# Kernel optimization log

Hardware: AMD Instinct MI355X
Metric: run time of the kernel (lower is better)

## Reference

```python
import jax, jax.numpy as jnp
import numpy as np

IN_DIM = 768
OUT_DIM = 4096
N_SK_ITER = 3
TARGET_TEMP = 0.06
PRED_TEMP = 0.12
PREFACTOR = 1.0
EXP_MAX = 50.0  # exp_max_values[float32]
SK_EPS = 1e-8
NORM_EPS = 1e-7


def setup_inputs() -> dict:
    key = jax.random.key(0)
    kx, kw = jax.random.split(key)
    x = jax.random.normal(kx, (16, 1024, IN_DIM), dtype=jnp.float32)
    # nn.Linear weight init: normal(std=1); bias zeros
    weight = jax.random.normal(kw, (OUT_DIM, IN_DIM), dtype=jnp.float32)
    bias = jnp.zeros((OUT_DIM,), dtype=jnp.float32)
    return {"x": x, "weight": weight, "bias": bias}


def sinkhorn_knopp(M, n_iterations, eps=SK_EPS):
    # stable_exp: shift by max over dim=-2 (token axis), add EXP_MAX
    shift = jnp.max(M, axis=-2, keepdims=True)
    M = jnp.exp(M + EXP_MAX - shift)
    for _ in range(n_iterations):  # small fixed count
        M = M / (jnp.sum(M, axis=-2, keepdims=True) + eps)  # column normalize
        M = M / (jnp.sum(M, axis=-1, keepdims=True) + eps)  # row normalize
    return M


def reference(x, weight, bias):
    # L2 normalize features (eps matches torch F.normalize with p=2)
    norm = jnp.maximum(jnp.linalg.norm(x, axis=-1, keepdims=True), NORM_EPS)
    x_n = x / norm
    logits = jnp.einsum("bnd,kd->bnk", x_n, weight) + bias  # [B, N, K]
    # positionwise_sk=True: no flatten before sinkhorn; detach -> stop_gradient
    assignments = sinkhorn_knopp(jax.lax.stop_gradient(logits) / TARGET_TEMP, N_SK_ITER)
    tgt = assignments.reshape(-1, OUT_DIM).astype(jnp.float32)
    pred = logits.reshape(-1, OUT_DIM).astype(jnp.float32)
    loss = -jnp.mean(jnp.sum(tgt * jax.nn.log_softmax(pred / PRED_TEMP, axis=-1), axis=-1))
    return assignments, PREFACTOR * loss
```

## Files before the change

kernel.cpp:

```cpp
#include <hip/hip_runtime.h>
#include <math.h>

#define BATCH 16
#define NTOK  1024
#define NCLU  4096
#define DIM   768
#define MROWS (BATCH * NTOK)

constexpr float TT_INV    = 16.666666666666668f;
constexpr float PT_INV    = 8.333333333333334f;
constexpr float SK_EPS_   = 1e-8f;
constexpr float NORM_EPS_ = 1e-7f;
constexpr float COL_SHIFT = 60.0f;
constexpr float P_SHIFT   = 40.0f;

typedef _Float16 f16x8 __attribute__((ext_vector_type(8)));
typedef _Float16 f16x4 __attribute__((ext_vector_type(4)));
typedef float    f32x4 __attribute__((ext_vector_type(4)));

struct F8 { float v[8]; };

__device__ __forceinline__ F8 load8(const float* p) {
    const float4 a = *(const float4*)p;
    const float4 b = *(const float4*)(p + 4);
    return F8{{a.x, a.y, a.z, a.w, b.x, b.y, b.z, b.w}};
}
__device__ __forceinline__ F8 load8(const _Float16* p) {
    f16x8 h = *(const f16x8*)p;
    F8 r;
#pragma unroll
    for (int i = 0; i < 8; ++i) r.v[i] = (float)h[i];
    return r;
}

__device__ __forceinline__ float wave_sum(float s) {
#pragma unroll
    for (int off = 32; off; off >>= 1) s += __shfl_xor(s, off);
    return s;
}

__device__ __forceinline__ void gl_lds16(const void* g, void* l) {
    __builtin_amdgcn_global_load_lds(
        (const __attribute__((address_space(1))) unsigned int*)g,
        (__attribute__((address_space(3))) unsigned int*)l,
        16, 0, 0);
}

__global__ __launch_bounds__(256) void castx_kernel(
    const float* __restrict__ x, _Float16* __restrict__ x16)
{
    int row  = (blockIdx.x * 256 + threadIdx.x) >> 6;
    int lane = threadIdx.x & 63;
    const float4* rp = (const float4*)(x + (size_t)row * DIM);
    float4 v[3];
    float ss = 0.f;
#pragma unroll
    for (int i = 0; i < 3; ++i) {
        v[i] = rp[lane + i * 64];
        ss += v[i].x * v[i].x + v[i].y * v[i].y + v[i].z * v[i].z + v[i].w * v[i].w;
    }
    ss = wave_sum(ss);
    float sc = 1.0f / fmaxf(sqrtf(ss), NORM_EPS_);
    _Float16* op = x16 + (size_t)row * DIM;
#pragma unroll
    for (int i = 0; i < 3; ++i) {
        f16x4 h;
        h[0] = (_Float16)(v[i].x * sc); h[1] = (_Float16)(v[i].y * sc);
        h[2] = (_Float16)(v[i].z * sc); h[3] = (_Float16)(v[i].w * sc);
        *(f16x4*)(op + 4 * (lane + i * 64)) = h;
    }
}

__global__ __launch_bounds__(256) void castw_kernel(
    const float* __restrict__ w, _Float16* __restrict__ w16)
{
    int i = blockIdx.x * 256 + threadIdx.x;
    const float4 a = *(const float4*)(w + (size_t)i * 8);
    const float4 b = *(const float4*)(w + (size_t)i * 8 + 4);
    f16x8 h;
    h[0] = (_Float16)a.x; h[1] = (_Float16)a.y; h[2] = (_Float16)a.z; h[3] = (_Float16)a.w;
    h[4] = (_Float16)b.x; h[5] = (_Float16)b.y; h[6] = (_Float16)b.z; h[7] = (_Float16)b.w;
    *(f16x8*)(w16 + (size_t)i * 8) = h;
}

__global__ __launch_bounds__(256) void rownorm_kernel(
    const float* __restrict__ x, float* __restrict__ invn)
{
    int wave = (blockIdx.x * 256 + threadIdx.x) >> 6;
    int lane = threadIdx.x & 63;
    const float4* row = (const float4*)(x + (size_t)wave * DIM);
    float s = 0.f;
#pragma unroll
    for (int i = 0; i < 3; ++i) {
        float4 v = row[lane + i * 64];
        s += v.x * v.x + v.y * v.y + v.z * v.z + v.w * v.w;
    }
    s = wave_sum(s);
    if (lane == 0) invn[wave] = 1.0f / fmaxf(sqrtf(s), NORM_EPS_);
}

#define GKH   32
#define NKH   (DIM / GKH)

__global__ void __launch_bounds__(512, 1) gemm16(
    const _Float16* __restrict__ A,
    const _Float16* __restrict__ B,
    const float* __restrict__ bias,
    _Float16* __restrict__ out,
    float* __restrict__ colpart)
{
    __shared__ __align__(16) _Float16 AS[4][8192];
    __shared__ __align__(16) _Float16 BS[4][8192];

    const int tid  = threadIdx.x;
    const int lane = tid & 63;
    const int wid  = tid >> 6;
    const int wm   = wid >> 2;
    const int wn   = wid & 3;

    const int nwg = gridDim.x;
    const int cpx = nwg >> 3;
    const int swz = (blockIdx.x & 7) * cpx + (blockIdx.x >> 3);
    const int brow = (swz >> 4) * 256;
    const int bcol = (swz & 15) * 256;

    const int G0 = tid, G1 = tid + 512;
    const int pr0 = G0 >> 3, s0 = G0 & 7;
    const int rr0 = pr0 * 2 + (s0 >> 2), qq0 = (s0 & 3) ^ (pr0 & 3);
    const int pr1 = G1 >> 3, s1 = G1 & 7;
    const int rr1 = pr1 * 2 + (s1 >> 2), qq1 = (s1 & 3) ^ (pr1 & 3);

    const _Float16* sA0 = A + (size_t)(brow + rr0) * DIM + qq0 * 8;
    const _Float16* sA1 = A + (size_t)(brow + rr1) * DIM + qq1 * 8;
    const _Float16* sB0 = B + (size_t)(bcol + rr0) * DIM + qq0 * 8;
    const _Float16* sB1 = B + (size_t)(bcol + rr1) * DIM + qq1 * 8;
    const int ldsOff0 = wid * 512;
    const int ldsOff1 = wid * 512 + 4096;

    const int q  = lane >> 4;
    const int fr = lane & 15;
    const int qp = q ^ ((fr >> 1) & 3);
    const int fbase = ((fr & 1) * 4 + qp) * 8;
    const int abase = (wm * 64 + (fr >> 1)) * 64 + fbase;
    const int bbase = (wn * 32 + (fr >> 1)) * 64 + fbase;

    f32x4 acc[8][4] = {};

#define STAGE4(slot, kh) {                                  \
    const int ko_ = (kh) * GKH;                             \
    gl_lds16(sA0 + ko_, &AS[slot][ldsOff0]);                \
    gl_lds16(sA1 + ko_, &AS[slot][ldsOff1]);                \
    gl_lds16(sB0 + ko_, &BS[slot][ldsOff0]);                \
    gl_lds16(sB1 + ko_, &BS[slot][ldsOff1]); }

#define PHASE(slotC, slotS, khS) {                                         \
    STAGE4(slotS, khS);                                                    \
    asm volatile("s_waitcnt vmcnt(8)" ::: "memory");                       \
    __builtin_amdgcn_s_barrier();                                          \
    asm volatile("" ::: "memory");                                         \
    f16x8 af[8], bf[4];                                                    \
    _Pragma("unroll")                                                      \
    for (int m = 0; m < 8; ++m)                                            \
        af[m] = *(const f16x8*)&AS[slotC][abase + m * 512];                \
    _Pragma("unroll")                                                      \
    for (int n = 0; n < 4; ++n)                                            \
        bf[n] = *(const f16x8*)&BS[slotC][bbase + n * 512];                \
    __builtin_amdgcn_s_setprio(1);                                         \
    _Pragma("unroll")                                                      \
    for (int m = 0; m < 8; ++m)                                            \
        _Pragma("unroll")                                                  \
        for (int n = 0; n < 4; ++n)                                        \
            acc[m][n] = __builtin_amdgcn_mfma_f32_16x16x32_f16(            \
                af[m], bf[n], acc[m][n], 0, 0, 0);                         \
    __builtin_amdgcn_s_setprio(0); }

    STAGE4(0, 0);
    STAGE4(1, 1);

    for (int i6 = 0; i6 < 6; ++i6) {
        const int i = i6 * 4;
        const int kh2 = i + 2;
        const int kh3 = i + 3;
        const int kh4 = (i + 4 < NKH) ? i + 4 : i + 4 - NKH;
        const int kh5 = (i + 5 < NKH) ? i + 5 : i + 5 - NKH;
        PHASE(0, 2, kh2);
        PHASE(1, 3, kh3);
        PHASE(2, 0, kh4);
        PHASE(3, 1, kh5);
    }
#undef PHASE
#undef STAGE4

    __syncthreads();

    float cs[4] = {0.f, 0.f, 0.f, 0.f};
    float bv[4];
#pragma unroll
    for (int n = 0; n < 4; ++n) bv[n] = bias[bcol + wn * 64 + n * 16 + fr];
#pragma unroll
    for (int m = 0; m < 8; ++m) {
        int row0 = brow + wm * 128 + m * 16 + (q << 2);
#pragma unroll
        for (int j = 0; j < 4; ++j) {
            size_t ro = (size_t)(row0 + j) * NCLU + bcol + wn * 64 + fr;
#pragma unroll
            for (int n = 0; n < 4; ++n) {
                float v = acc[m][n][j] + bv[n];
                out[ro + n * 16] = (_Float16)v;
                cs[n] += __expf(v * TT_INV - COL_SHIFT);
            }
        }
    }
    float cred_local[4];
#pragma unroll
    for (int n = 0; n < 4; ++n) {
        float c2 = cs[n];
        c2 += __shfl_xor(c2, 16);
        c2 += __shfl_xor(c2, 32);
        cred_local[n] = c2;
    }
    float* cred = (float*)&AS[0][0];
#pragma unroll
    for (int n = 0; n < 4; ++n)
        if (q == 0) cred[((wm * 4 + wn) * 4 + n) * 16 + fr] = cred_local[n];
    __syncthreads();
    if (tid < 256) {
        int wn2 = tid >> 6, n2 = (tid >> 4) & 3, fr2 = tid & 15;
        float S = cred[((0 * 4 + wn2) * 4 + n2) * 16 + fr2]
                + cred[((1 * 4 + wn2) * 4 + n2) * 16 + fr2];
        colpart[(size_t)(swz >> 4) * NCLU + bcol + wn2 * 64 + n2 * 16 + fr2] = S;
    }
}

__global__ __launch_bounds__(256) void colfin_kernel(
    const float* __restrict__ part, float* __restrict__ a1)
{
    int i = blockIdx.x * 256 + threadIdx.x;
    int b = i >> 12, k = i & (NCLU - 1);
    const float* p = part + (size_t)(b * 4) * NCLU + k;
    float s = 0.f;
#pragma unroll
    for (int rb = 0; rb < 4; ++rb) { s += *p; p += NCLU; }
    a1[i] = -COL_SHIFT - __logf(s);
}

template <bool FIRST>
__global__ __launch_bounds__(256) void rcpass_kernel(
    const _Float16* __restrict__ L, const float* __restrict__ a_in,
    const float* __restrict__ b_in, float* __restrict__ b_out,
    float* __restrict__ part)
{
    __shared__ float wgt_sh[16];
    const int tid  = threadIdx.x;
    const int lane = tid & 63;
    const int wv   = tid >> 6;
    const int chunk = blockIdx.x;
    const int b     = chunk >> 6;
    const int row0  = chunk * 16;
    const float* av = a_in + (size_t)b * NCLU;

    float ar[8][8];
#pragma unroll
    for (int i = 0; i < 8; ++i) {
        int c = i * 64 + lane;
        *(float4*)&ar[i][0] = *(const float4*)&av[c * 8];
        *(float4*)&ar[i][4] = *(const float4*)&av[c * 8 + 4];
    }

#pragma unroll
    for (int rr = 0; rr < 4; ++rr) {
        int row = row0 + wv * 4 + rr;
        const _Float16* Lr = L + (size_t)row * NCLU;
        float bp = FIRST ? 0.f : b_in[row];
        float s = 0.f;
#pragma unroll
        for (int i = 0; i < 8; ++i) {
            int c = i * 64 + lane;
            f16x8 h = *(const f16x8*)&Lr[c * 8];
#pragma unroll
            for (int j = 0; j < 8; ++j)
                s += __expf((float)h[j] * TT_INV + ar[i][j] + bp);
        }
        s = wave_sum(s);
        if (lane == 0) {
            float bn = bp - __logf(s + SK_EPS_);
            b_out[row] = bn;
            wgt_sh[wv * 4 + rr] = __expf(bn);
        }
    }
    __syncthreads();

    float aown[2][8];
#pragma unroll
    for (int sl = 0; sl < 2; ++sl) {
        *(float4*)&aown[sl][0] = *(const float4*)&av[sl * 2048 + tid * 8];
        *(float4*)&aown[sl][4] = *(const float4*)&av[sl * 2048 + tid * 8 + 4];
    }
    float acc[2][8] = {};
    for (int rr = 0; rr < 16; ++rr) {
        const _Float16* Lr = L + (size_t)(row0 + rr) * NCLU;
        float wg = wgt_sh[rr];
#pragma unroll
        for (int sl = 0; sl < 2; ++sl) {
            f16x8 h = *(const f16x8*)&Lr[sl * 2048 + tid * 8];
#pragma unroll
            for (int j = 0; j < 8; ++j)
                acc[sl][j] += __expf((float)h[j] * TT_INV + aown[sl][j]) * wg;
        }
    }
    float* P = part + (size_t)chunk * NCLU;
#pragma unroll
    for (int sl = 0; sl < 2; ++sl) {
        f32x4 w0, w1;
        w0[0] = acc[sl][0]; w0[1] = acc[sl][1]; w0[2] = acc[sl][2]; w0[3] = acc[sl][3];
        w1[0] = acc[sl][4]; w1[1] = acc[sl][5]; w1[2] = acc[sl][6]; w1[3] = acc[sl][7];
        *(f32x4*)&P[sl * 2048 + tid * 8]     = w0;
        *(f32x4*)&P[sl * 2048 + tid * 8 + 4] = w1;
    }
}

__global__ __launch_bounds__(256) void colfinN_kernel(
    const float* __restrict__ part, const float* __restrict__ a_in,
    float* __restrict__ a_out)
{
    int i = blockIdx.x * 256 + threadIdx.x;
    int b = i >> 12, k = i & (NCLU - 1);
    const float* p = part + (size_t)(b * 64) * NCLU + k;
    float s = 0.f;
#pragma unroll 8
    for (int c = 0; c < 64; ++c) { s += *p; p += NCLU; }
    a_out[i] = a_in[i] - __logf(s + SK_EPS_);
}

#define BM 128
#define BN 128
#define BKF 32
#define LDK 40

__device__ __forceinline__ f16x8 pack8(float4 lo, float4 hi, float sc) {
    f16x8 h;
    h[0] = (_Float16)(lo.x * sc); h[1] = (_Float16)(lo.y * sc);
    h[2] = (_Float16)(lo.z * sc); h[3] = (_Float16)(lo.w * sc);
    h[4] = (_Float16)(hi.x * sc); h[5] = (_Float16)(hi.y * sc);
    h[6] = (_Float16)(hi.z * sc); h[7] = (_Float16)(hi.w * sc);
    return h;
}

template <typename OT>
__global__ __launch_bounds__(256) void gemm_f16(
    const float* __restrict__ x, const float* __restrict__ w,
    const float* __restrict__ bias, const float* __restrict__ invn,
    OT* __restrict__ out)
{
    __shared__ __align__(16) _Float16 As[BM * LDK];
    __shared__ __align__(16) _Float16 Bs[BN * LDK];

    const int tid  = threadIdx.x;
    const int lane = tid & 63;
    const int wid  = tid >> 6;
    const int wr = wid >> 1, wc = wid & 1;
    const int brow = blockIdx.y * BM;
    const int bcol = blockIdx.x * BN;

    const int r0 = tid >> 2;
    const int r1 = r0 + 64;
    const int kc = (tid & 3) * 8;
    const float sA0 = invn[brow + r0];
    const float sA1 = invn[brow + r1];
    const float* gA0 = x + (size_t)(brow + r0) * DIM + kc;
    const float* gA1 = x + (size_t)(brow + r1) * DIM + kc;
    const float* gB0 = w + (size_t)(bcol + r0) * DIM + kc;
    const float* gB1 = w + (size_t)(bcol + r1) * DIM + kc;

    f32x4 acc[4][4] = {};
    float4 a00, a01, a10, a11, b00, b01, b10, b11;
    a00 = *(const float4*)(gA0);     a01 = *(const float4*)(gA0 + 4);
    a10 = *(const float4*)(gA1);     a11 = *(const float4*)(gA1 + 4);
    b00 = *(const float4*)(gB0);     b01 = *(const float4*)(gB0 + 4);
    b10 = *(const float4*)(gB1);     b11 = *(const float4*)(gB1 + 4);

    const int NT = DIM / BKF;
    for (int kt = 0; kt < NT; ++kt) {
        __syncthreads();
        *(f16x8*)&As[r0 * LDK + kc] = pack8(a00, a01, sA0);
        *(f16x8*)&As[r1 * LDK + kc] = pack8(a10, a11, sA1);
        *(f16x8*)&Bs[r0 * LDK + kc] = pack8(b00, b01, 1.0f);
        *(f16x8*)&Bs[r1 * LDK + kc] = pack8(b10, b11, 1.0f);
        __syncthreads();

        if (kt + 1 < NT) {
            int k0 = (kt + 1) * BKF;
            a00 = *(const float4*)(gA0 + k0); a01 = *(const float4*)(gA0 + k0 + 4);
            a10 = *(const float4*)(gA1 + k0); a11 = *(const float4*)(gA1 + k0 + 4);
            b00 = *(const float4*)(gB0 + k0); b01 = *(const float4*)(gB0 + k0 + 4);
            b10 = *(const float4*)(gB1 + k0); b11 = *(const float4*)(gB1 + k0 + 4);
        }

        const int ko = (lane >> 4) * 8;
        f16x8 af[4], bf[4];
#pragma unroll
        for (int m = 0; m < 4; ++m)
            af[m] = *(const f16x8*)&As[(wr * 64 + m * 16 + (lane & 15)) * LDK + ko];
#pragma unroll
        for (int n = 0; n < 4; ++n)
            bf[n] = *(const f16x8*)&Bs[(wc * 64 + n * 16 + (lane & 15)) * LDK + ko];
#pragma unroll
        for (int m = 0; m < 4; ++m)
#pragma unroll
            for (int n = 0; n < 4; ++n)
                acc[m][n] = __builtin_amdgcn_mfma_f32_16x16x32_f16(
                    af[m], bf[n], acc[m][n], 0, 0, 0);
    }

#pragma unroll
    for (int n = 0; n < 4; ++n) {
        int col = bcol + wc * 64 + n * 16 + (lane & 15);
        float bv = bias[col];
#pragma unroll
        for (int m = 0; m < 4; ++m) {
            int row0 = brow + wr * 64 + m * 16 + ((lane >> 4) << 2);
#pragma unroll
            for (int j = 0; j < 4; ++j)
                out[(size_t)(row0 + j) * NCLU + col] = (OT)(acc[m][n][j] + bv);
        }
    }
}

template <typename T>
__global__ __launch_bounds__(256) void colpass_kernel(
    const T* __restrict__ L, const float* __restrict__ a_in,
    const float* __restrict__ b_in, float* __restrict__ a_out)
{
    __shared__ float bsh[NTOK];
    __shared__ float ss[4][64];
    int b = blockIdx.x >> 6;
    int k = ((blockIdx.x & 63) << 6) + (threadIdx.x & 63);
    int wv = threadIdx.x >> 6;
    int lane = threadIdx.x & 63;
    const bool first = (b_in == nullptr);
    if (first) {
        for (int i = threadIdx.x; i < NTOK; i += 256) bsh[i] = 0.f;
    } else {
        for (int i = threadIdx.x; i < NTOK; i += 256) bsh[i] = b_in[b * NTOK + i];
    }
    __syncthreads();
    float aval = first ? -COL_SHIFT : a_in[b * NCLU + k];
    const T* p = L + (size_t)b * NTOK * NCLU + (size_t)(wv * 256) * NCLU + k;
    float s = 0.f;
#pragma unroll 4
    for (int n = 0; n < 256; ++n) {
        s += __expf((float)(*p) * TT_INV + aval + bsh[wv * 256 + n]);
        p += NCLU;
    }
    ss[wv][lane] = s;
    __syncthreads();
    if (wv == 0) {
        float S = ss[0][lane] + ss[1][lane] + ss[2][lane] + ss[3][lane];
        a_out[b * NCLU + k] = aval - __logf(first ? S : S + SK_EPS_);
    }
}

template <typename T>
__global__ __launch_bounds__(256) void colpassV_kernel(
    const T* __restrict__ L, const float* __restrict__ a_in,
    const float* __restrict__ b_in, float* __restrict__ a_out)
{
    __shared__ float bsh[NTOK];
    __shared__ float red[16][16][8];
    const int b     = blockIdx.x >> 5;
    const int strip = blockIdx.x & 31;
    const int cc    = threadIdx.x & 15;
    const int rg    = threadIdx.x >> 4;
    const int col0  = strip * 128 + cc * 8;
    for (int i = threadIdx.x; i < NTOK; i += 256) bsh[i] = b_in[b * NTOK + i];
    __syncthreads();
    const float4 av0 = *(const float4*)(a_in + b * NCLU + col0);
    const float4 av1 = *(const float4*)(a_in + b * NCLU + col0 + 4);
    const float av[8] = {av0.x, av0.y, av0.z, av0.w, av1.x, av1.y, av1.z, av1.w};
    float s[8] = {};
    const T* p = L + (size_t)b * NTOK * NCLU + (size_t)rg * NCLU + col0;
    for (int it = 0; it < 64; ++it) {
        F8 Lv = load8(p);
        float bpv = bsh[it * 16 + rg];
#pragma unroll
        for (int j = 0; j < 8; ++j) s[j] += __expf(Lv.v[j] * TT_INV + av[j] + bpv);
        p += (size_t)16 * NCLU;
    }
#pragma unroll
    for (int j = 0; j < 8; ++j) red[rg][cc][j] = s[j];
    __syncthreads();
    if (threadIdx.x < 128) {
        int c2 = threadIdx.x >> 3, j2 = threadIdx.x & 7;
        float S = 0.f;
#pragma unroll
        for (int g = 0; g < 16; ++g) S += red[g][c2][j2];
        int col = strip * 128 + c2 * 8 + j2;
        a_out[b * NCLU + col] = a_in[b * NCLU + col] - __logf(S + SK_EPS_);
    }
}

template <typename T>
__global__ __launch_bounds__(256) void rowpass_kernel(
    const T* __restrict__ L, const float* __restrict__ a_in,
    const float* __restrict__ b_in, float* __restrict__ b_out)
{
    int row  = (blockIdx.x * 256 + threadIdx.x) >> 6;
    int lane = threadIdx.x & 63;
    int b = row >> 10;
    const T* Lr = L + (size_t)row * NCLU;
    const float* av = a_in + (size_t)b * NCLU;
    float bp = b_in ? b_in[row] : 0.f;
    float s = 0.f;
#pragma unroll
    for (int i = 0; i < 8; ++i) {
        int c = i * 64 + lane;
        F8 Lv = load8(Lr + c * 8);
        F8 Av = load8(av + c * 8);
#pragma unroll
        for (int j = 0; j < 8; ++j)
            s += __expf(Lv.v[j] * TT_INV + Av.v[j] + bp);
    }
    s = wave_sum(s);
    if (lane == 0) b_out[row] = bp - __logf(s + SK_EPS_);
}

template <typename T>
__global__ __launch_bounds__(256) void final_kernel(
    const T* __restrict__ L, const float* __restrict__ a3,
    const float* __restrict__ b2, float* __restrict__ out,
    float* __restrict__ rowloss)
{
    __shared__ float red[3][4];
    const int row  = blockIdx.x;
    const int tid  = threadIdx.x;
    const int lane = tid & 63;
    const int wv   = tid >> 6;
    const int b    = row >> 10;
    const T* Lr = L + (size_t)row * NCLU;
    const float* av = a3 + (size_t)b * NCLU;
    const float bp = b2[row];

    float e[2][8];
    float rs = 0.f, q = 0.f, sP = 0.f;
#pragma unroll
    for (int jj = 0; jj < 2; ++jj) {
        int c = tid + jj * 256;
        F8 Lv = load8(Lr + c * 8);
        F8 Av = load8(av + c * 8);
#pragma unroll
        for (int j = 0; j < 8; ++j) {
            float P  = Lv.v[j] * PT_INV;
            float ev = __expf(Lv.v[j] * TT_INV + Av.v[j] + bp);
            e[jj][j] = ev;
            rs += ev;
            q  += ev * P;
            sP += __expf(P - P_SHIFT);
        }
    }
    rs = wave_sum(rs); q = wave_sum(q); sP = wave_sum(sP);
    if (lane == 0) { red[0][wv] = rs; red[1][wv] = q; red[2][wv] = sP; }
    __syncthreads();
    rs = red[0][0] + red[0][1] + red[0][2] + red[0][3];
    q  = red[1][0] + red[1][1] + red[1][2] + red[1][3];
    sP = red[2][0] + red[2][1] + red[2][2] + red[2][3];

    const float inv = 1.0f / (rs + SK_EPS_);
    const float lse = P_SHIFT + __logf(sP);

    float* Or = out + (size_t)row * NCLU;
#pragma unroll
    for (int jj = 0; jj < 2; ++jj) {
        int c = tid + jj * 256;
        f32x4 w0, w1;
        w0[0] = e[jj][0] * inv; w0[1] = e[jj][1] * inv;
        w0[2] = e[jj][2] * inv; w0[3] = e[jj][3] * inv;
        w1[0] = e[jj][4] * inv; w1[1] = e[jj][5] * inv;
        w1[2] = e[jj][6] * inv; w1[3] = e[jj][7] * inv;
        __builtin_nontemporal_store(w0, (f32x4*)(Or + c * 8));
        __builtin_nontemporal_store(w1, (f32x4*)(Or + c * 8 + 4));
    }
    if (tid == 0) rowloss[row] = q * inv - lse * (rs * inv);
}

__global__ __launch_bounds__(256) void lossred_kernel(
    const float* __restrict__ rowloss, float* __restrict__ out_loss)
{
    __shared__ float red[4];
    int tid = threadIdx.x, lane = tid & 63, wv = tid >> 6;
    float s = 0.f;
    for (int i = tid; i < MROWS; i += 256) s += rowloss[i];
    s = wave_sum(s);
    if (lane == 0) red[wv] = s;
    __syncthreads();
    if (tid == 0)
        out_loss[0] = -(red[0] + red[1] + red[2] + red[3]) / (float)MROWS;
}

extern "C" void kernel_launch(void* const* d_in, const int* in_sizes, int n_in,
                              void* d_out, int out_size, void* d_ws, size_t ws_size,
                              hipStream_t stream)
{
    const float* x    = (const float*)d_in[0];
    const float* w    = (const float*)d_in[1];
    const float* bias = (const float*)d_in[2];
    float* out = (float*)d_out;
    char* base = (char*)d_ws;
    float* ws  = (float*)d_ws;

    float* a1      = ws;
    float* a2      = a1 + BATCH * NCLU;
    float* a3      = a2 + BATCH * NCLU;
    float* b1      = a3 + BATCH * NCLU;
    float* b2      = b1 + MROWS;
    float* rowloss = b2 + MROWS;

    const size_t SMALL = 1u << 20;
    const size_t L16B  = (size_t)MROWS * NCLU * 2;
    const size_t X16B  = (size_t)MROWS * DIM * 2;
    const size_t W16B  = (size_t)NCLU * DIM * 2;
    const size_t PARTB = (size_t)64 * NCLU * 4;

    const int CB = BATCH * (NCLU / 64);
    const int RB = MROWS / 4;

    if (ws_size >= SMALL + L16B + X16B + W16B + PARTB) {
        _Float16* L16 = (_Float16*)(base + SMALL);
        _Float16* X16 = (_Float16*)(base + SMALL + L16B);
        _Float16* W16 = (_Float16*)(base + SMALL + L16B + X16B);
        float*    part1 = (float*)(base + SMALL + L16B + X16B + W16B);
        float*    part  = (float*)(base + SMALL + L16B);

        castx_kernel<<<MROWS / 4, 256, 0, stream>>>(x, X16);
        castw_kernel<<<(NCLU * DIM / 8) / 256, 256, 0, stream>>>(w, W16);
        gemm16<<<(MROWS / 256) * (NCLU / 256), 512, 0, stream>>>(X16, W16, bias, L16, part1);
        colfin_kernel<<<BATCH * NCLU / 256, 256, 0, stream>>>(part1, a1);
        rcpass_kernel<true ><<<MROWS / 16, 256, 0, stream>>>(L16, a1, nullptr, b1, part);
        colfinN_kernel<<<BATCH * NCLU / 256, 256, 0, stream>>>(part, a1, a2);
        rcpass_kernel<false><<<MROWS / 16, 256, 0, stream>>>(L16, a2, b1, b2, part);
        colfinN_kernel<<<BATCH * NCLU / 256, 256, 0, stream>>>(part, a2, a3);
        final_kernel<_Float16><<<MROWS, 256, 0, stream>>>(L16, a3, b2, out, rowloss);
        lossred_kernel<<<1, 256, 0, stream>>>(rowloss, out + (size_t)MROWS * NCLU);
    } else if (ws_size >= SMALL + L16B) {
        float* invn = rowloss + MROWS;
        _Float16* L16 = (_Float16*)(base + SMALL);
        rownorm_kernel<<<MROWS / 4, 256, 0, stream>>>(x, invn);
        dim3 gg(NCLU / BN, MROWS / BM);
        gemm_f16<_Float16><<<gg, 256, 0, stream>>>(x, w, bias, invn, L16);
        colpass_kernel<_Float16><<<CB, 256, 0, stream>>>(L16, nullptr, nullptr, a1);
        rowpass_kernel<_Float16><<<RB, 256, 0, stream>>>(L16, a1, nullptr, b1);
        colpassV_kernel<_Float16><<<BATCH * 32, 256, 0, stream>>>(L16, a1, b1, a2);
        rowpass_kernel<_Float16><<<RB, 256, 0, stream>>>(L16, a2, b1, b2);
        colpassV_kernel<_Float16><<<BATCH * 32, 256, 0, stream>>>(L16, a2, b2, a3);
        final_kernel<_Float16><<<MROWS, 256, 0, stream>>>(L16, a3, b2, out, rowloss);
        lossred_kernel<<<1, 256, 0, stream>>>(rowloss, out + (size_t)MROWS * NCLU);
    } else {
        float* invn = rowloss + MROWS;
        rownorm_kernel<<<MROWS / 4, 256, 0, stream>>>(x, invn);
        dim3 gg(NCLU / BN, MROWS / BM);
        gemm_f16<float><<<gg, 256, 0, stream>>>(x, w, bias, invn, out);
        colpass_kernel<float><<<CB, 256, 0, stream>>>(out, nullptr, nullptr, a1);
        rowpass_kernel<float><<<RB, 256, 0, stream>>>(out, a1, nullptr, b1);
        colpassV_kernel<float><<<BATCH * 32, 256, 0, stream>>>(out, a1, b1, a2);
        rowpass_kernel<float><<<RB, 256, 0, stream>>>(out, a2, b1, b2);
        colpassV_kernel<float><<<BATCH * 32, 256, 0, stream>>>(out, a2, b2, a3);
        final_kernel<float><<<MROWS, 256, 0, stream>>>(out, a3, b2, out, rowloss);
        lossred_kernel<<<1, 256, 0, stream>>>(rowloss, out + (size_t)MROWS * NCLU);
    }
}
```

Baseline: 321.7 us.

## Stage row chunk in LDS to avoid re-reading L in column pass

The row/column Sinkhorn pass now copies each 16-row chunk of the fp16 logits into a 128 KB shared-memory buffer during the row-sum phase. The column-partial phase then reads from LDS instead of reloading the chunk from global memory. Block size is doubled to 512 threads, so each thread owns a single 8-column slice and each wave handles two rows instead of four. The large LDS footprint limits occupancy to roughly one block per CU, which may reduce latency hiding.

Measured after the change: 319.6 us. About the same (-0.6%).

```diff
diff --git a/kernel.cpp b/kernel.cpp
--- a/kernel.cpp
+++ b/kernel.cpp
@@ -245,11 +245,12 @@
 }
 
 template <bool FIRST>
-__global__ __launch_bounds__(256) void rcpass_kernel(
+__global__ void __launch_bounds__(512, 1) rcpassL_kernel(
     const _Float16* __restrict__ L, const float* __restrict__ a_in,
     const float* __restrict__ b_in, float* __restrict__ b_out,
     float* __restrict__ part)
 {
+    __shared__ __align__(16) _Float16 Lsh[16][NCLU];
     __shared__ float wgt_sh[16];
     const int tid  = threadIdx.x;
     const int lane = tid & 63;
@@ -268,8 +269,9 @@
     }
 
 #pragma unroll
-    for (int rr = 0; rr < 4; ++rr) {
-        int row = row0 + wv * 4 + rr;
+    for (int rr = 0; rr < 2; ++rr) {
+        int lr  = wv * 2 + rr;
+        int row = row0 + lr;
         const _Float16* Lr = L + (size_t)row * NCLU;
         float bp = FIRST ? 0.f : b_in[row];
         float s = 0.f;
@@ -277,6 +279,7 @@
         for (int i = 0; i < 8; ++i) {
             int c = i * 64 + lane;
             f16x8 h = *(const f16x8*)&Lr[c * 8];
+            *(f16x8*)&Lsh[lr][c * 8] = h;
 #pragma unroll
             for (int j = 0; j < 8; ++j)
                 s += __expf((float)h[j] * TT_INV + ar[i][j] + bp);
@@ -285,38 +288,28 @@
         if (lane == 0) {
             float bn = bp - __logf(s + SK_EPS_);
             b_out[row] = bn;
-            wgt_sh[wv * 4 + rr] = __expf(bn);
+            wgt_sh[lr] = __expf(bn);
         }
     }
     __syncthreads();
 
-    float aown[2][8];
-#pragma unroll
-    for (int sl = 0; sl < 2; ++sl) {
-        *(float4*)&aown[sl][0] = *(const float4*)&av[sl * 2048 + tid * 8];
-        *(float4*)&aown[sl][4] = *(const float4*)&av[sl * 2048 + tid * 8 + 4];
-    }
-    float acc[2][8] = {};
+    float aown[8];
+    *(float4*)&aown[0] = *(const float4*)&av[tid * 8];
+    *(float4*)&aown[4] = *(const float4*)&av[tid * 8 + 4];
+    float acc[8] = {};
     for (int rr = 0; rr < 16; ++rr) {
-        const _Float16* Lr = L + (size_t)(row0 + rr) * NCLU;
+        f16x8 h = *(const f16x8*)&Lsh[rr][tid * 8];
         float wg = wgt_sh[rr];
 #pragma unroll
-        for (int sl = 0; sl < 2; ++sl) {
-            f16x8 h = *(const f16x8*)&Lr[sl * 2048 + tid * 8];
-#pragma unroll
-            for (int j = 0; j < 8; ++j)
-                acc[sl][j] += __expf((float)h[j] * TT_INV + aown[sl][j]) * wg;
-        }
+        for (int j = 0; j < 8; ++j)
+            acc[j] += __expf((float)h[j] * TT_INV + aown[j]) * wg;
     }
     float* P = part + (size_t)chunk * NCLU;
-#pragma unroll
-    for (int sl = 0; sl < 2; ++sl) {
-        f32x4 w0, w1;
-        w0[0] = acc[sl][0]; w0[1] = acc[sl][1]; w0[2] = acc[sl][2]; w0[3] = acc[sl][3];
-        w1[0] = acc[sl][4]; w1[1] = acc[sl][5]; w1[2] = acc[sl][6]; w1[3] = acc[sl][7];
-        *(f32x4*)&P[sl * 2048 + tid * 8]     = w0;
-        *(f32x4*)&P[sl * 2048 + tid * 8 + 4] = w1;
-    }
+    f32x4 w0, w1;
+    w0[0] = acc[0]; w0[1] = acc[1]; w0[2] = acc[2]; w0[3] = acc[3];
+    w1[0] = acc[4]; w1[1] = acc[5]; w1[2] = acc[6]; w1[3] = acc[7];
+    *(f32x4*)&P[tid * 8]     = w0;
+    *(f32x4*)&P[tid * 8 + 4] = w1;
 }
 
 __global__ __launch_bounds__(256) void colfinN_kernel(
@@ -634,9 +627,9 @@
         castw_kernel<<<(NCLU * DIM / 8) / 256, 256, 0, stream>>>(w, W16);
         gemm16<<<(MROWS / 256) * (NCLU / 256), 512, 0, stream>>>(X16, W16, bias, L16, part1);
         colfin_kernel<<<BATCH * NCLU / 256, 256, 0, stream>>>(part1, a1);
-        rcpass_kernel<true ><<<MROWS / 16, 256, 0, stream>>>(L16, a1, nullptr, b1, part);
+        rcpassL_kernel<true ><<<MROWS / 16, 512, 0, stream>>>(L16, a1, nullptr, b1, part);
         colfinN_kernel<<<BATCH * NCLU / 256, 256, 0, stream>>>(part, a1, a2);
-        rcpass_kernel<false><<<MROWS / 16, 256, 0, stream>>>(L16, a2, b1, b2, part);
+        rcpassL_kernel<false><<<MROWS / 16, 512, 0, stream>>>(L16, a2, b1, b2, part);
         colfinN_kernel<<<BATCH * NCLU / 256, 256, 0, stream>>>(part, a2, a3);
         final_kernel<_Float16><<<MROWS, 256, 0, stream>>>(L16, a3, b2, out, rowloss);
         lossred_kernel<<<1, 256, 0, stream>>>(rowloss, out + (size_t)MROWS * NCLU);
```
